# Optimization experiments

Hardware: AMD Instinct MI355X
Metric: run time of the kernel (lower is better)

Reference implementation:

```python
import jax, jax.numpy as jnp
import numpy as np

SQRT3 = float(np.sqrt(3.0))
TWO_PI = float(2.0 * np.pi)


def _safe_sqrt(x):
    return jnp.sqrt(jnp.clip(x, 1e-5))


def _matern(Q):
    # Matern 3/2 on the (already halved) quadratic form, matching torch matern()
    t = SQRT3 * _safe_sqrt(Q)
    return (1.0 + t) * jnp.exp(-t)


def _pairwise_kernel(x1, kp1, x2, kp2, scale):
    """Fused prob_product_quad + prob_product_constant + matern.

    x: [B,N,2] coords; kp: [B,N,3] = (e00, e11, e01) of SPD 2x2 E per point.
    Returns K [B,N,M].
    """
    a1, b1, c1 = kp1[..., 0], kp1[..., 1], kp1[..., 2]  # e00, e11, e01
    a2, b2, c2 = kp2[..., 0], kp2[..., 1], kp2[..., 2]
    det1 = a1 * b1 - c1 * c1  # det2x2(E1) [B,N]
    det2 = a2 * b2 - c2 * c2  # [B,M]
    s00 = a1[:, :, None] + a2[:, None, :]  # E1_00 + E2_00  [B,N,M]
    s11 = b1[:, :, None] + b2[:, None, :]
    s01 = c1[:, :, None] + c2[:, None, :]
    sdet = s00 * s11 - s01 * s01  # det(E1+E2)
    d = x1[:, :, None, :] - x2[:, None, :, :]  # [B,N,M,2]
    d0, d1 = d[..., 0], d[..., 1]
    Q = (s11 * d0 * d0 - 2.0 * s01 * d0 * d1 + s00 * d1 * d1) / sdet * 0.5
    C = 2.0 * (det1 ** 0.25)[:, :, None] * (det2 ** 0.25)[:, None, :] / _safe_sqrt(sdet)
    return _matern(Q) * C * scale


def _diag_kernel(kp, scale):
    # diagonal_prob_product: Q = 0, C = 2*sqrt(det E)/safe_sqrt(det(2E))
    a, b, c = kp[..., 0], kp[..., 1], kp[..., 2]
    det = a * b - c * c
    det2E = 4.0 * det  # det(2E) for 2x2
    C = 2.0 * jnp.sqrt(det) / _safe_sqrt(det2E)
    Q = jnp.zeros_like(C)
    return C * _matern(Q) * scale  # [B,N]


def setup_inputs() -> dict:
    key = jax.random.key(0)
    ks = jax.random.split(key, 8)
    B, N, M = 2, 1024, 16384

    def kparams(k, n):
        u = jax.random.uniform(k, (B, n, 3), dtype=jnp.float32)
        a = 0.5 + u[..., 0]
        b = 0.5 + u[..., 1]
        c = 0.2 * (u[..., 2] - 0.5)  # |c| small -> SPD
        return jnp.stack([a, b, c], axis=-1)

    coords_train = jax.random.uniform(ks[0], (B, N, 2), dtype=jnp.float32) * 512.0 / 64.0
    coords_test = jax.random.uniform(ks[1], (B, M, 2), dtype=jnp.float32) * 512.0 / 64.0
    kernel_params_train = kparams(ks[2], N)
    kernel_params_test = kparams(ks[3], M)
    y_train = jax.random.uniform(ks[4], (B, N, 1), dtype=jnp.float32) * 10.0
    var = 0.01 + 0.1 * jax.random.uniform(ks[5], (B, N), dtype=jnp.float32)
    mean = jnp.zeros((B, 1, 1), dtype=jnp.float32)
    scale_param = jnp.zeros((1,), dtype=jnp.float32)
    return {
        "coords_train": coords_train,
        "kernel_params_train": kernel_params_train,
        "coords_test": coords_test,
        "kernel_params_test": kernel_params_test,
        "y_train": y_train,
        "var": var,
        "mean": mean,
        "scale_param": scale_param,
    }


def reference(coords_train, kernel_params_train, coords_test, kernel_params_test,
              y_train, var, mean, scale_param):
    scale_prior = 1.0
    scale = scale_prior * jnp.exp(scale_param[0])  # CovarianceModule.get_scale
    B, N = coords_train.shape[0], coords_train.shape[1]

    # CovarianceModule / CrossCovarianceModule / DiagonalCovarianceModule
    K_nn = _pairwise_kernel(coords_train, kernel_params_train,
                            coords_train, kernel_params_train, scale)  # [B,N,N]
    K_nm = _pairwise_kernel(coords_train, kernel_params_train,
                            coords_test, kernel_params_test, scale)    # [B,N,M]
    K_mm_diag = _diag_kernel(kernel_params_test, scale)                 # [B,M]

    # GpSparseModule: A = K_nn + diag(var); chol; alpha = A^{-1}(y-mean); NLML
    eye = jnp.eye(N, dtype=K_nn.dtype)
    A = K_nn + var[..., None] * eye
    L = jnp.linalg.cholesky(A)
    y_centered = y_train - mean
    alpha = jax.scipy.linalg.cho_solve((L, True), y_centered)  # [B,N,1]
    data_fit = jnp.sum(y_centered * alpha, axis=1)             # [B,1]
    data_term = 0.5 * jnp.sum(data_fit, axis=1)                # [B]
    complexity_term = jnp.sum(jnp.log(jnp.diagonal(L, axis1=-2, axis2=-1)), axis=1)
    constant_term = 0.5 * N * np.log(TWO_PI)
    nlml = data_term + complexity_term + constant_term

    # GpDenseModule: predictive mean/variance at test points
    pred_mean = mean + jnp.einsum('bnm,bnk->bmk', K_nm, alpha)  # [B,M,1]
    v = jax.scipy.linalg.cho_solve((L, True), K_nm)             # [B,N,M]
    pred_var = (K_mm_diag - jnp.sum(K_nm * v, axis=1))[..., None]  # [B,M,1]
    return pred_mean, pred_var, nlml
```

## Files before the change

kernel.cpp:

```cpp
#include <hip/hip_runtime.h>
#include <math.h>

namespace {
constexpr int kB = 2;
constexpr int kN = 1024;
constexpr int kM = 16384;
constexpr float kSqrt3 = 1.7320508075688772f;

constexpr size_t A_BYTES = (size_t)kB * kN * kN * 4;
constexpr size_t DG_BYTES = (size_t)kB * 8 * 128 * 128 * 4;
constexpr size_t Z_BYTES = (size_t)kB * kN * 4;
constexpr size_t LH_BYTES = (size_t)kB * kN * kN * 2;
constexpr size_t DH_BYTES = (size_t)kB * 8 * 128 * 128 * 2;
constexpr size_t A_OFF = 0;
constexpr size_t DG_OFF = A_OFF + A_BYTES;
constexpr size_t Z_OFF = DG_OFF + DG_BYTES;
constexpr size_t LH_OFF = Z_OFF + Z_BYTES;
constexpr size_t LL_OFF = LH_OFF + LH_BYTES;
constexpr size_t DH_OFF = LL_OFF + LH_BYTES;
constexpr size_t DL_OFF = DH_OFF + DH_BYTES;
constexpr size_t WS_BYTES = DL_OFF + DH_BYTES;
}

typedef __attribute__((ext_vector_type(8))) short short8v;
typedef __attribute__((ext_vector_type(4))) float floatx4;

__device__ __forceinline__ float b16f(unsigned short h) {
  return __uint_as_float(((unsigned)h) << 16);
}
__device__ __forceinline__ unsigned short b16rn(float x) {
  unsigned u = __float_as_uint(x);
  unsigned r = u + 0x7FFFu + ((u >> 16) & 1u);
  return (unsigned short)(r >> 16);
}
__device__ __forceinline__ void split_bf16(float x, unsigned short& h, unsigned short& l) {
  unsigned u = __float_as_uint(x);
  h = (unsigned short)(u >> 16);
  float rem = x - b16f(h);
  l = (unsigned short)(__float_as_uint(rem) >> 16);
}
__device__ __forceinline__ void pack2(float v0, float v1, unsigned& hw, unsigned& lw) {
  unsigned u0 = __float_as_uint(v0), u1 = __float_as_uint(v1);
  unsigned h0 = u0 & 0xFFFF0000u;
  unsigned h1 = u1 & 0xFFFF0000u;
  hw = (h0 >> 16) | h1;
  float r0 = v0 - __uint_as_float(h0);
  float r1 = v1 - __uint_as_float(h1);
  lw = (__float_as_uint(r0) >> 16) | (__float_as_uint(r1) & 0xFFFF0000u);
}

__device__ __forceinline__ float pair_kernel(
    float x0, float x1, float a1, float b1, float c1,
    float y0, float y1, float a2, float b2, float c2, float scale) {
  float det1 = a1 * b1 - c1 * c1;
  float det2 = a2 * b2 - c2 * c2;
  float s00 = a1 + a2, s11 = b1 + b2, s01 = c1 + c2;
  float sdet = s00 * s11 - s01 * s01;
  float rsq = rsqrtf(fmaxf(sdet, 1e-5f));
  float d0 = x0 - y0, d1 = x1 - y1;
  float quad = s11 * d0 * d0 - 2.0f * s01 * d0 * d1 + s00 * d1 * d1;
  float u = 1.5f * quad * rsq * rsq;
  float t = sqrtf(fmaxf(u, 3e-5f));
  float C = 2.0f * sqrtf(sqrtf(det1)) * sqrtf(sqrtf(det2)) * rsq;
  return (1.0f + t) * __expf(-t) * C * scale;
}

__global__ __launch_bounds__(256) void build_A(
    const float* __restrict__ xt, const float* __restrict__ pt,
    const float* __restrict__ var, const float* __restrict__ sp,
    float* __restrict__ A) {
  int idx = blockIdx.x * 256 + threadIdx.x;
  int b = idx / (kN * kN);
  int r = (idx / kN) % kN;
  int c = idx % kN;
  float scale = __expf(sp[0]);
  const float* x1 = xt + ((size_t)b * kN + r) * 2;
  const float* p1 = pt + ((size_t)b * kN + r) * 3;
  const float* x2 = xt + ((size_t)b * kN + c) * 2;
  const float* p2 = pt + ((size_t)b * kN + c) * 3;
  float k = pair_kernel(x1[0], x1[1], p1[0], p1[1], p1[2],
                        x2[0], x2[1], p2[0], p2[1], p2[2], scale);
  if (r == c) k += var[b * kN + r];
  A[(size_t)idx] = k;
}

__device__ __forceinline__ void tri_decode(int idx, int& ti, int& tj) {
  float f = sqrtf(8.0f * (float)idx + 1.0f);
  int t0 = (int)((f - 1.0f) * 0.5f);
  while (t0 * (t0 + 1) / 2 > idx) --t0;
  while ((t0 + 1) * (t0 + 2) / 2 <= idx) ++t0;
  ti = t0;
  tj = idx - t0 * (t0 + 1) / 2;
}

__global__ __launch_bounds__(1024, 1) void chol_panel(float* __restrict__ A,
                                                      float* __restrict__ Dg,
                                                      unsigned short* __restrict__ Dh,
                                                      unsigned short* __restrict__ Dl, int p) {
  __shared__ float At[128 * 132];
  __shared__ float Dt[128 * 132];
  __shared__ float Tt[3 * 32 * 33];
  int b = blockIdx.x, t = threadIdx.x;
  float* Ab = A + (size_t)b * kN * kN;
  int r0 = p * 128;
#pragma unroll
  for (int q = 0; q < 4; ++q) {
    int idx = t + 1024 * q;
    int r = idx >> 5, c4 = idx & 31;
    *(float4*)&At[r * 132 + c4 * 4] = *(const float4*)&Ab[(size_t)(r0 + r) * kN + r0 + c4 * 4];
  }
  __syncthreads();
  int wave = t >> 6, lane = t & 63;
  int row0 = lane, row1 = lane + 64;
  for (int kb = 0; kb < 16; ++kb) {
    int K0 = kb * 8;
    int Kp = K0 - 8;
    if (kb > 0) {
      if (wave == 0) {
        int rr = lane >> 3, cc = lane & 7;
        float s = 0.0f;
#pragma unroll
        for (int e = 0; e < 8; ++e)
          s += At[(K0 + rr) * 132 + Kp + e] * At[(K0 + cc) * 132 + Kp + e];
        At[(K0 + rr) * 132 + K0 + cc] -= s;
      } else {
        int n = 120 - 8 * kb;
        int nt = n >> 2;
        int ntt = nt * (nt + 1) / 2;
        int base = K0 + 8;
        for (int idx = t - 64; idx < ntt; idx += 960) {
          int ti, tj;
          tri_decode(idx, ti, tj);
          int i0 = base + ti * 4, j0 = base + tj * 4;
          float Li[4][8], Lj[4][8];
#pragma unroll
          for (int r = 0; r < 4; ++r) {
            *(float4*)&Li[r][0] = *(const float4*)&At[(i0 + r) * 132 + Kp];
            *(float4*)&Li[r][4] = *(const float4*)&At[(i0 + r) * 132 + Kp + 4];
            *(float4*)&Lj[r][0] = *(const float4*)&At[(j0 + r) * 132 + Kp];
            *(float4*)&Lj[r][4] = *(const float4*)&At[(j0 + r) * 132 + Kp + 4];
          }
#pragma unroll
          for (int r = 0; r < 4; ++r) {
            float4 cv = *(const float4*)&At[(i0 + r) * 132 + j0];
            float cc4[4] = {cv.x, cv.y, cv.z, cv.w};
#pragma unroll
            for (int c = 0; c < 4; ++c) {
              float s = 0.0f;
#pragma unroll
              for (int e = 0; e < 8; ++e) s += Li[r][e] * Lj[c][e];
              cc4[c] -= s;
            }
            float4 ov = {cc4[0], cc4[1], cc4[2], cc4[3]};
            *(float4*)&At[(i0 + r) * 132 + j0] = ov;
          }
        }
      }
    }
    __syncthreads();
    if (wave == 0) {
      float rA0[8], rA1[8];
      *(float4*)&rA0[0] = *(const float4*)&At[row0 * 132 + K0];
      *(float4*)&rA0[4] = *(const float4*)&At[row0 * 132 + K0 + 4];
      *(float4*)&rA1[0] = *(const float4*)&At[row1 * 132 + K0];
      *(float4*)&rA1[4] = *(const float4*)&At[row1 * 132 + K0 + 4];
      if (kb > 0) {
        float pA0[8], pA1[8];
        *(float4*)&pA0[0] = *(const float4*)&At[row0 * 132 + Kp];
        *(float4*)&pA0[4] = *(const float4*)&At[row0 * 132 + Kp + 4];
        *(float4*)&pA1[0] = *(const float4*)&At[row1 * 132 + Kp];
        *(float4*)&pA1[4] = *(const float4*)&At[row1 * 132 + Kp + 4];
#pragma unroll
        for (int j = 0; j < 8; ++j) {
          float s0 = 0.0f, s1 = 0.0f;
#pragma unroll
          for (int e = 0; e < 8; ++e) {
            float pj = At[(K0 + j) * 132 + Kp + e];
            s0 += pA0[e] * pj;
            s1 += pA1[e] * pj;
          }
          rA0[j] -= s0;
          rA1[j] -= s1;
        }
      }
      float L11[8][8], idg[8];
#pragma unroll
      for (int r = 0; r < 8; ++r) {
        *(float4*)&L11[r][0] = *(const float4*)&At[(K0 + r) * 132 + K0];
        *(float4*)&L11[r][4] = *(const float4*)&At[(K0 + r) * 132 + K0 + 4];
      }
#pragma unroll
      for (int c = 0; c < 8; ++c) {
        float d = sqrtf(L11[c][c]);
        float iv = 1.0f / d;
        idg[c] = iv;
        L11[c][c] = d;
#pragma unroll
        for (int i = c + 1; i < 8; ++i) L11[i][c] *= iv;
#pragma unroll
        for (int j = c + 1; j < 8; ++j)
#pragma unroll
          for (int i = j; i < 8; ++i) L11[i][j] -= L11[i][c] * L11[j][c];
      }
      if (row0 >= K0 + 8) {
#pragma unroll
        for (int c = 0; c < 8; ++c) {
          float s = rA0[c];
#pragma unroll
          for (int j = 0; j < c; ++j) s -= rA0[j] * L11[c][j];
          rA0[c] = s * idg[c];
        }
      } else if (row0 >= K0) {
#pragma unroll
        for (int rr = 0; rr < 8; ++rr)
          if (row0 - K0 == rr) {
#pragma unroll
            for (int e = 0; e < 8; ++e) rA0[e] = (e <= rr) ? L11[rr][e] : 0.0f;
          }
      }
      if (row1 >= K0 + 8) {
#pragma unroll
        for (int c = 0; c < 8; ++c) {
          float s = rA1[c];
#pragma unroll
          for (int j = 0; j < c; ++j) s -= rA1[j] * L11[c][j];
          rA1[c] = s * idg[c];
        }
      } else if (row1 >= K0) {
#pragma unroll
        for (int rr = 0; rr < 8; ++rr)
          if (row1 - K0 == rr) {
#pragma unroll
            for (int e = 0; e < 8; ++e) rA1[e] = (e <= rr) ? L11[rr][e] : 0.0f;
          }
      }
      if (row0 >= K0) {
        float4 v0 = {rA0[0], rA0[1], rA0[2], rA0[3]};
        float4 v1 = {rA0[4], rA0[5], rA0[6], rA0[7]};
        *(float4*)&At[row0 * 132 + K0] = v0;
        *(float4*)&At[row0 * 132 + K0 + 4] = v1;
      }
      if (row1 >= K0) {
        float4 v0 = {rA1[0], rA1[1], rA1[2], rA1[3]};
        float4 v1 = {rA1[4], rA1[5], rA1[6], rA1[7]};
        *(float4*)&At[row1 * 132 + K0] = v0;
        *(float4*)&At[row1 * 132 + K0 + 4] = v1;
      }
    }
    __syncthreads();
  }
  if (t < 128) {
    int q = t >> 5, c = t & 31, bse = q * 32;
    float x[32];
#pragma unroll
    for (int r = 0; r < 32; ++r) {
      float s = (r == c) ? 1.0f : 0.0f;
#pragma unroll
      for (int j = 0; j < 32; ++j)
        if (j < r) s -= At[(bse + r) * 132 + bse + j] * x[j];
      x[r] = (r < c) ? 0.0f : s / At[(bse + r) * 132 + bse + r];
    }
#pragma unroll
    for (int r = 0; r < 32; ++r) Dt[(bse + r) * 132 + bse + c] = x[r];
  }
  __syncthreads();
  {
    int r = t >> 5, cl = t & 31;
    for (int s = 1; s <= 3; ++s) {
      for (int blk = 0; blk < 4 - s; ++blk) {
        int J = blk, I = J + s;
        float sum = 0.0f;
        for (int K = J; K < I; ++K)
          for (int j = 0; j < 32; ++j)
            sum += At[(I * 32 + r) * 132 + K * 32 + j] * Dt[(K * 32 + j) * 132 + J * 32 + cl];
        Tt[blk * (32 * 33) + r * 33 + cl] = sum;
      }
      __syncthreads();
      for (int blk = 0; blk < 4 - s; ++blk) {
        int J = blk, I = J + s;
        float sum = 0.0f;
        for (int j = 0; j < 32; ++j)
          sum += Dt[(I * 32 + r) * 132 + I * 32 + j] * Tt[blk * (32 * 33) + j * 33 + cl];
        Dt[(I * 32 + r) * 132 + J * 32 + cl] = -sum;
      }
      __syncthreads();
    }
  }
#pragma unroll
  for (int q = 0; q < 4; ++q) {
    int jj = t + 1024 * q;
    int r = jj >> 5, ch = jj & 31;
    int c0 = ch * 4;
    float4 v = *(const float4*)&At[r * 132 + c0];
    v.x = (c0 + 0 <= r) ? v.x : 0.0f;
    v.y = (c0 + 1 <= r) ? v.y : 0.0f;
    v.z = (c0 + 2 <= r) ? v.z : 0.0f;
    v.w = (c0 + 3 <= r) ? v.w : 0.0f;
    *(float4*)&Ab[(size_t)(r0 + r) * kN + r0 + c0] = v;
  }
  float* Db = Dg + (size_t)(b * 8 + p) * 16384;
  unsigned short* Dhb = Dh + (size_t)(b * 8 + p) * 16384;
  unsigned short* Dlb = Dl + (size_t)(b * 8 + p) * 16384;
#pragma unroll
  for (int q = 0; q < 4; ++q) {
    int jj = t + 1024 * q;
    int r = jj >> 5, ch = jj & 31;
    int c0 = ch * 4;
    float4 v = *(const float4*)&Dt[r * 132 + c0];
    v.x = (c0 + 0 <= r) ? v.x : 0.0f;
    v.y = (c0 + 1 <= r) ? v.y : 0.0f;
    v.z = (c0 + 2 <= r) ? v.z : 0.0f;
    v.w = (c0 + 3 <= r) ? v.w : 0.0f;
    *(float4*)&Db[r * 128 + c0] = v;
    float vv[4] = {v.x, v.y, v.z, v.w};
    unsigned short hs[4], ls[4];
#pragma unroll
    for (int e = 0; e < 4; ++e) split_bf16(vv[e], hs[e], ls[e]);
    *(ushort4*)&Dhb[r * 128 + c0] = make_ushort4(hs[0], hs[1], hs[2], hs[3]);
    *(ushort4*)&Dlb[r * 128 + c0] = make_ushort4(ls[0], ls[1], ls[2], ls[3]);
  }
}

__global__ __launch_bounds__(256) void chol_trsm(float* __restrict__ A,
                                                 const float* __restrict__ Dg,
                                                 unsigned short* __restrict__ Lh, int p) {
  __shared__ float At[128 * 129];
  __shared__ float Dt[128 * 129];
  int b = blockIdx.y, rb = blockIdx.x;
  int rs = (p + 1 + rb) * 128;
  float* Ab = A + (size_t)b * kN * kN;
  const float* Db = Dg + (size_t)(b * 8 + p) * 16384;
  int t = threadIdx.x;
  for (int q = 0; q < 64; ++q) {
    int li = t + 256 * q;
    int r = li >> 7, cc = li & 127;
    At[r * 129 + cc] = Ab[(size_t)(rs + r) * kN + p * 128 + cc];
    Dt[r * 129 + cc] = Db[r * 128 + cc];
  }
  __syncthreads();
  int tx = t & 15, ty = t >> 4;
  float acc[8][8] = {};
  for (int j = 0; j < 128; ++j) {
    float a[8], d[8];
#pragma unroll
    for (int q = 0; q < 8; ++q) a[q] = At[(ty * 8 + q) * 129 + j];
#pragma unroll
    for (int q = 0; q < 8; ++q) d[q] = Dt[(tx * 8 + q) * 129 + j];
#pragma unroll
    for (int qr = 0; qr < 8; ++qr)
#pragma unroll
      for (int qc = 0; qc < 8; ++qc) acc[qr][qc] = fmaf(a[qr], d[qc], acc[qr][qc]);
  }
#pragma unroll
  for (int qr = 0; qr < 8; ++qr)
#pragma unroll
    for (int qc = 0; qc < 8; ++qc) {
      float v = acc[qr][qc];
      Ab[(size_t)(rs + ty * 8 + qr) * kN + p * 128 + tx * 8 + qc] = v;
      size_t lo = ((size_t)b * kN + rs + ty * 8 + qr) * kN + p * 128 + tx * 8 + qc;
      Lh[lo] = b16rn(-v);
    }
}

__global__ __launch_bounds__(256) void chol_syrk(float* __restrict__ A, int p) {
  __shared__ float L1t[128 * 129];
  __shared__ float L2t[128 * 129];
  int b = blockIdx.y;
  int pid = blockIdx.x;
  int bi = 0;
  while ((bi + 1) * (bi + 2) / 2 <= pid) ++bi;
  int bj = pid - bi * (bi + 1) / 2;
  int rs1 = (p + 1 + bi) * 128, rs2 = (p + 1 + bj) * 128;
  float* Ab = A + (size_t)b * kN * kN;
  int t = threadIdx.x;
  for (int q = 0; q < 64; ++q) {
    int li = t + 256 * q;
    int r = li >> 7, cc = li & 127;
    L1t[r * 129 + cc] = Ab[(size_t)(rs1 + r) * kN + p * 128 + cc];
    L2t[r * 129 + cc] = Ab[(size_t)(rs2 + r) * kN + p * 128 + cc];
  }
  __syncthreads();
  int tx = t & 15, ty = t >> 4;
  float acc[8][8] = {};
  for (int j = 0; j < 128; ++j) {
    float a[8], d[8];
#pragma unroll
    for (int q = 0; q < 8; ++q) a[q] = L1t[(ty * 8 + q) * 129 + j];
#pragma unroll
    for (int q = 0; q < 8; ++q) d[q] = L2t[(tx * 8 + q) * 129 + j];
#pragma unroll
    for (int qr = 0; qr < 8; ++qr)
#pragma unroll
      for (int qc = 0; qc < 8; ++qc) acc[qr][qc] = fmaf(a[qr], d[qc], acc[qr][qc]);
  }
#pragma unroll
  for (int qr = 0; qr < 8; ++qr)
#pragma unroll
    for (int qc = 0; qc < 8; ++qc) {
      size_t o = (size_t)(rs1 + ty * 8 + qr) * kN + rs2 + tx * 8 + qc;
      Ab[o] -= acc[qr][qc];
    }
}

__global__ __launch_bounds__(1024) void solve_small(
    const float* __restrict__ A, const float* __restrict__ Dg,
    const float* __restrict__ y, const float* __restrict__ meanp,
    float* __restrict__ zbuf, float* __restrict__ out) {
  __shared__ float Ls[128 * 132];
  __shared__ __align__(16) float zs[1024];
  __shared__ float ts[128];
  __shared__ float part[128 * 9];
  __shared__ float red[1024];
  int b = blockIdx.x, t = threadIdx.x;
  int row = t & 127, g = t >> 7;
  const float* Ab = A + (size_t)b * kN * kN;
  float mv = meanp[b];
  zs[t] = y[b * kN + t] - mv;
  __syncthreads();
  for (int i = 0; i < 8; ++i) {
    float ps = 0.0f;
    for (int k = 0; k < i; ++k) {
#pragma unroll
      for (int q = 0; q < 4; ++q) {
        int li = t + 1024 * q;
        int r = li >> 5, c4 = li & 31;
        *(float4*)&Ls[r * 132 + c4 * 4] =
            *(const float4*)&Ab[(size_t)(i * 128 + r) * kN + k * 128 + c4 * 4];
      }
      __syncthreads();
      const float* Lr = &Ls[row * 132 + g * 16];
      const float* zk = &zs[k * 128 + g * 16];
#pragma unroll
      for (int c = 0; c < 16; c += 4) {
        float4 lv = *(const float4*)&Lr[c];
        float4 zv = *(const float4*)&zk[c];
        ps += lv.x * zv.x + lv.y * zv.y + lv.z * zv.z + lv.w * zv.w;
      }
      __syncthreads();
    }
    part[row * 9 + g] = ps;
    {
      const float* Db = Dg + (size_t)(b * 8 + i) * 16384;
#pragma unroll
      for (int q = 0; q < 4; ++q) {
        int li = t + 1024 * q;
        int r = li >> 5, c4 = li & 31;
        *(float4*)&Ls[r * 132 + c4 * 4] = *(const float4*)&Db[r * 128 + c4 * 4];
      }
    }
    __syncthreads();
    if (g == 0) {
      float acc = zs[i * 128 + row];
#pragma unroll
      for (int gg = 0; gg < 8; ++gg) acc -= part[row * 9 + gg];
      ts[row] = acc;
    }
    __syncthreads();
    float s = 0.0f;
    int c0 = g * 16, c1 = min(c0 + 16, row + 1);
    for (int c = c0; c < c1; ++c) s += Ls[row * 132 + c] * ts[c];
    part[row * 9 + g] = s;
    __syncthreads();
    if (g == 0) {
      float zv = 0.0f;
#pragma unroll
      for (int gg = 0; gg < 8; ++gg) zv += part[row * 9 + gg];
      zs[i * 128 + row] = zv;
    }
    __syncthreads();
  }
  red[t] = zs[t] * zs[t];
  __syncthreads();
  for (int s = 512; s > 0; s >>= 1) {
    if (t < s) red[t] += red[t + s];
    __syncthreads();
  }
  float dfs = red[0];
  __syncthreads();
  red[t] = logf(Ab[(size_t)t * kN + t]);
  __syncthreads();
  for (int s = 512; s > 0; s >>= 1) {
    if (t < s) red[t] += red[t + s];
    __syncthreads();
  }
  if (t == 0)
    out[2 * kB * kM + b] = 0.5f * dfs + red[0] + 0.5f * 1024.0f * logf(6.283185307179586f);
  zbuf[b * kN + t] = zs[t];
}

__global__ __launch_bounds__(256, 2) void fused_mfma(
    const unsigned short* __restrict__ Lh,
    const unsigned short* __restrict__ Dh, const unsigned short* __restrict__ Dl,
    const float* __restrict__ xt, const float* __restrict__ pt,
    const float* __restrict__ xs, const float* __restrict__ ps,
    const float* __restrict__ sp, const float* __restrict__ meanp,
    const float* __restrict__ zbuf, float* __restrict__ out) {
  __shared__ unsigned short Th[32 * 136];
  __shared__ unsigned short Tl[32 * 136];
  __shared__ float trp2[2][128 * 6];
  __shared__ float zs2[2][128];
  __shared__ float tp[32 * 6];
  __shared__ float red[32 * 16 * 2];
  int bid = blockIdx.x;
  int xcd = bid & 7;
  int b = xcd >> 2;
  int mt = (xcd & 3) * 128 + (bid >> 3);
  int t = threadIdx.x;
  int lane = t & 63, wave = t >> 6;
  int lrow = lane & 15, kgrp = lane >> 4;
  float scale = __expf(sp[0]);
  if (t < 32) {
    int mg = mt * 32 + t;
    float x0 = xs[((size_t)b * kM + mg) * 2 + 0];
    float x1 = xs[((size_t)b * kM + mg) * 2 + 1];
    float a = ps[((size_t)b * kM + mg) * 3 + 0];
    float bb = ps[((size_t)b * kM + mg) * 3 + 1];
    float c = ps[((size_t)b * kM + mg) * 3 + 2];
    float det2 = a * bb - c * c;
    tp[t * 6 + 0] = x0; tp[t * 6 + 1] = x1; tp[t * 6 + 2] = a;
    tp[t * 6 + 3] = bb; tp[t * 6 + 4] = c; tp[t * 6 + 5] = sqrtf(sqrtf(det2));
  }
  if (t < 128) {
    size_t n = (size_t)b * kN + t;
    float x0 = xt[n * 2 + 0];
    float x1 = xt[n * 2 + 1];
    float a = pt[n * 3 + 0];
    float bb = pt[n * 3 + 1];
    float c = pt[n * 3 + 2];
    float det1 = a * bb - c * c;
    trp2[0][t * 6 + 0] = x0; trp2[0][t * 6 + 1] = x1; trp2[0][t * 6 + 2] = a;
    trp2[0][t * 6 + 3] = bb; trp2[0][t * 6 + 4] = c;
    trp2[0][t * 6 + 5] = 2.0f * scale * sqrtf(sqrtf(det1));
    zs2[0][t] = zbuf[n];
  }
  floatx4 W[8][2][2];
#pragma unroll
  for (int i = 0; i < 8; ++i)
#pragma unroll
    for (int rf = 0; rf < 2; ++rf)
#pragma unroll
      for (int cf = 0; cf < 2; ++cf) W[i][rf][cf] = (floatx4){0.f, 0.f, 0.f, 0.f};
  float pma[2] = {0.f, 0.f}, s2a[2] = {0.f, 0.f};
  __syncthreads();

#define FUSED_K_STEP(KC)                                                                   \
  {                                                                                        \
    constexpr int k = (KC);                                                                \
    const float* trp = trp2[k & 1];                                                        \
                                                           \
    _Pragma("unroll")                                                                      \
    for (int rf = 0; rf < 2; ++rf) {                                                       \
      int n0 = wave * 32 + rf * 16 + kgrp * 4;                                             \
      float nx0[4], nx1[4], na[4], nb[4], nc[4], nc1[4];                                   \
      _Pragma("unroll")                                                                    \
      for (int r = 0; r < 4; ++r) {                                                        \
        int n = n0 + r;                                                                    \
        nx0[r] = trp[n * 6 + 0]; nx1[r] = trp[n * 6 + 1]; na[r] = trp[n * 6 + 2];          \
        nb[r] = trp[n * 6 + 3]; nc[r] = trp[n * 6 + 4]; nc1[r] = trp[n * 6 + 5];           \
      }                                                                                    \
      _Pragma("unroll")                                                                    \
      for (int cf = 0; cf < 2; ++cf) {                                                     \
        int m = cf * 16 + lrow;                                                            \
        float mx0 = tp[m * 6 + 0], mx1 = tp[m * 6 + 1], ma = tp[m * 6 + 2];                \
        float mb = tp[m * 6 + 3], mc = tp[m * 6 + 4], mq = tp[m * 6 + 5];                  \
        float Tv[4];                                                                       \
        _Pragma("unroll")                                                                  \
        for (int r = 0; r < 4; ++r) {                                                      \
          float s00 = na[r] + ma, s11 = nb[r] + mb, s01 = nc[r] + mc;                      \
          float sdet = s00 * s11 - s01 * s01;                                              \
          float rsq = rsqrtf(fmaxf(sdet, 1e-5f));                                          \
          float d0 = nx0[r] - mx0, d1 = nx1[r] - mx1;                                      \
          float quad = s11 * d0 * d0 - 2.0f * s01 * d0 * d1 + s00 * d1 * d1;               \
          float u = 1.5f * quad * rsq * rsq;                                               \
          float tt = sqrtf(fmaxf(u, 3e-5f));                                               \
          float Kv = (1.0f + tt) * __expf(-tt) * nc1[r] * (mq * rsq);                      \
          Tv[r] = Kv + W[k][rf][cf][r];                                                    \
        }                                                                                  \
        unsigned hw[2], lw[2];                                                             \
        pack2(Tv[0], Tv[1], hw[0], lw[0]);                                                 \
        pack2(Tv[2], Tv[3], hw[1], lw[1]);                                                 \
        int off = m * 136 + n0;                                                            \
        *(uint2*)&Th[off] = make_uint2(hw[0], hw[1]);                                      \
        *(uint2*)&Tl[off] = make_uint2(lw[0], lw[1]);                                      \
      }                                                                                    \
    }                                                                                      \
    __syncthreads();                                                                \
                                 \
    if (k < 7 && t < 128) {                                                                \
      size_t n = (size_t)b * kN + (k + 1) * 128 + t;                                       \
      float x0 = xt[n * 2 + 0];                                                            \
      float x1 = xt[n * 2 + 1];                                                            \
      float a = pt[n * 3 + 0];                                                             \
      float bb = pt[n * 3 + 1];                                                            \
      float c = pt[n * 3 + 2];                                                             \
      float det1 = a * bb - c * c;                                                         \
      trp2[(k + 1) & 1][t * 6 + 0] = x0; trp2[(k + 1) & 1][t * 6 + 1] = x1;                \
      trp2[(k + 1) & 1][t * 6 + 2] = a;  trp2[(k + 1) & 1][t * 6 + 3] = bb;                \
      trp2[(k + 1) & 1][t * 6 + 4] = c;                                                    \
      trp2[(k + 1) & 1][t * 6 + 5] = 2.0f * scale * sqrtf(sqrtf(det1));                    \
      zs2[(k + 1) & 1][t] = zbuf[n];                                                       \
    }                                                                                      \
    floatx4 wk[2][2];                                                                      \
    _Pragma("unroll")                                                                      \
    for (int rf = 0; rf < 2; ++rf)                                                         \
      _Pragma("unroll")                                                                    \
      for (int cf = 0; cf < 2; ++cf) wk[rf][cf] = (floatx4){0.f, 0.f, 0.f, 0.f};           \
    {                                                                                      \
      const unsigned short* Dhb = Dh + (size_t)(b * 8 + k) * 16384;                        \
      const unsigned short* Dlb = Dl + (size_t)(b * 8 + k) * 16384;                        \
      _Pragma("unroll")                                                                    \
      for (int ks = 0; ks < 4; ++ks) {                                                     \
        short8v bh[2], bl[2];                                                              \
        _Pragma("unroll")                                                                  \
        for (int cf = 0; cf < 2; ++cf) {                                                   \
          int boff = (cf * 16 + lrow) * 136 + ks * 32 + kgrp * 8;                          \
          bh[cf] = *(const short8v*)&Th[boff];                                             \
          bl[cf] = *(const short8v*)&Tl[boff];                                             \
        }                                                                                  \
        short8v ah[2], al[2];                                                              \
        _Pragma("unroll")                                                                  \
        for (int rf = 0; rf < 2; ++rf) {                                                   \
          size_t aoff = (size_t)(wave * 32 + rf * 16 + lrow) * 128 + ks * 32 + kgrp * 8;   \
          ah[rf] = *(const short8v*)&Dhb[aoff];                                            \
          al[rf] = *(const short8v*)&Dlb[aoff];                                            \
        }                                                                                  \
        _Pragma("unroll")                                                                  \
        for (int rf = 0; rf < 2; ++rf)                                                     \
          _Pragma("unroll")                                                                \
          for (int cf = 0; cf < 2; ++cf) {                                                 \
            wk[rf][cf] = __builtin_amdgcn_mfma_f32_16x16x32_bf16(ah[rf], bh[cf], wk[rf][cf], 0, 0, 0); \
            wk[rf][cf] = __builtin_amdgcn_mfma_f32_16x16x32_bf16(ah[rf], bl[cf], wk[rf][cf], 0, 0, 0); \
            wk[rf][cf] = __builtin_amdgcn_mfma_f32_16x16x32_bf16(al[rf], bh[cf], wk[rf][cf], 0, 0, 0); \
          }                                                                                \
      }                                                                                    \
    }                                                                                      \
    __syncthreads();                                                                \
                                               \
    _Pragma("unroll")                                                                      \
    for (int rf = 0; rf < 2; ++rf) {                                                       \
      int n0 = wave * 32 + rf * 16 + kgrp * 4;                                             \
      _Pragma("unroll")                                                                    \
      for (int cf = 0; cf < 2; ++cf) {                                                     \
        int m = cf * 16 + lrow;                                                            \
        float wv[4];                                                                       \
        _Pragma("unroll")                                                                  \
        for (int r = 0; r < 4; ++r) {                                                      \
          wv[r] = wk[rf][cf][r];                                                           \
          pma[cf] = fmaf(wv[r], zs2[k & 1][n0 + r], pma[cf]);                              \
          s2a[cf] = fmaf(wv[r], wv[r], s2a[cf]);                                           \
        }                                                                                  \
        unsigned hw[2], lw[2];                                                             \
        pack2(wv[0], wv[1], hw[0], lw[0]);                                                 \
        pack2(wv[2], wv[3], hw[1], lw[1]);                                                 \
        int off = m * 136 + n0;                                                            \
        *(uint2*)&Th[off] = make_uint2(hw[0], hw[1]);                                      \
        *(uint2*)&Tl[off] = make_uint2(lw[0], lw[1]);                                      \
      }                                                                                    \
    }                                                                                      \
    __syncthreads();                                                                \
                                                            \
    __builtin_amdgcn_s_setprio(1);                                                         \
    _Pragma("unroll")                                                                      \
    for (int ks = 0; ks < 4; ++ks) {                                                       \
      short8v bh[2], bl[2];                                                                \
      _Pragma("unroll")                                                                    \
      for (int cf = 0; cf < 2; ++cf) {                                                     \
        int boff = (cf * 16 + lrow) * 136 + ks * 32 + kgrp * 8;                            \
        bh[cf] = *(const short8v*)&Th[boff];                                               \
        bl[cf] = *(const short8v*)&Tl[boff];                                               \
      }                                                                                    \
      _Pragma("unroll")                                                                    \
      for (int i = k + 1; i < 8; ++i) {                                                    \
        short8v ah[2];                                                                     \
        _Pragma("unroll")                                                                  \
        for (int rf = 0; rf < 2; ++rf) {                                                   \
          size_t ro = (size_t)b * kN + i * 128 + wave * 32 + rf * 16 + lrow;               \
          size_t aoff = ro * kN + k * 128 + ks * 32 + kgrp * 8;                            \
          ah[rf] = *(const short8v*)&Lh[aoff];                                             \
        }                                                                                  \
        _Pragma("unroll")                                                                  \
        for (int rf = 0; rf < 2; ++rf)                                                     \
          _Pragma("unroll")                                                                \
          for (int cf = 0; cf < 2; ++cf) {                                                 \
            W[i][rf][cf] = __builtin_amdgcn_mfma_f32_16x16x32_bf16(ah[rf], bh[cf], W[i][rf][cf], 0, 0, 0); \
            W[i][rf][cf] = __builtin_amdgcn_mfma_f32_16x16x32_bf16(ah[rf], bl[cf], W[i][rf][cf], 0, 0, 0); \
          }                                                                                \
      }                                                                                    \
    }                                                                                      \
    __builtin_amdgcn_s_setprio(0);                                                         \
    __syncthreads();             \
  }

  FUSED_K_STEP(0)
  FUSED_K_STEP(1)
  FUSED_K_STEP(2)
  FUSED_K_STEP(3)
  FUSED_K_STEP(4)
  FUSED_K_STEP(5)
  FUSED_K_STEP(6)
  FUSED_K_STEP(7)
#undef FUSED_K_STEP

#pragma unroll
  for (int cf = 0; cf < 2; ++cf) {
    int m = cf * 16 + lrow;
    red[m * 16 + wave * 4 + kgrp] = pma[cf];
    red[512 + m * 16 + wave * 4 + kgrp] = s2a[cf];
  }
  __syncthreads();
  if (t < 32) {
    float pm = 0.f, s2 = 0.f;
#pragma unroll
    for (int j = 0; j < 16; ++j) {
      pm += red[t * 16 + j];
      s2 += red[512 + t * 16 + j];
    }
    int mg = mt * 32 + t;
    float a = tp[t * 6 + 2], bb = tp[t * 6 + 3], c = tp[t * 6 + 4];
    float det = a * bb - c * c;
    float C = 2.0f * sqrtf(det) * rsqrtf(fmaxf(4.0f * det, 1e-5f));
    float t0 = kSqrt3 * sqrtf(1e-5f);
    float mat = (1.0f + t0) * __expf(-t0);
    float kd = C * mat * scale;
    out[b * kM + mg] = meanp[b] + pm;
    out[kB * kM + b * kM + mg] = kd - s2;
  }
}

extern "C" void kernel_launch(void* const* d_in, const int* in_sizes, int n_in,
                              void* d_out, int out_size, void* d_ws, size_t ws_size,
                              hipStream_t stream) {
  const float* xt = (const float*)d_in[0];
  const float* pt = (const float*)d_in[1];
  const float* xs = (const float*)d_in[2];
  const float* ps = (const float*)d_in[3];
  const float* y = (const float*)d_in[4];
  const float* var = (const float*)d_in[5];
  const float* meanp = (const float*)d_in[6];
  const float* sp = (const float*)d_in[7];
  float* out = (float*)d_out;
  char* ws = (char*)d_ws;
  if (ws_size < WS_BYTES) return;

  float* A = (float*)(ws + A_OFF);
  float* Dg = (float*)(ws + DG_OFF);
  float* zbuf = (float*)(ws + Z_OFF);
  unsigned short* Lh = (unsigned short*)(ws + LH_OFF);
  unsigned short* Dh = (unsigned short*)(ws + DH_OFF);
  unsigned short* Dl = (unsigned short*)(ws + DL_OFF);

  build_A<<<(kB * kN * kN) / 256, 256, 0, stream>>>(xt, pt, var, sp, A);
  for (int p = 0; p < 8; ++p) {
    chol_panel<<<kB, 1024, 0, stream>>>(A, Dg, Dh, Dl, p);
    if (p < 7) {
      int nt = 7 - p;
      chol_trsm<<<dim3(nt, kB), 256, 0, stream>>>(A, Dg, Lh, p);
      chol_syrk<<<dim3(nt * (nt + 1) / 2, kB), 256, 0, stream>>>(A, p);
    }
  }
  solve_small<<<kB, 1024, 0, stream>>>(A, Dg, y, meanp, zbuf, out);
  fused_mfma<<<kB * 512, 256, 0, stream>>>(Lh, Dh, Dl, xt, pt, xs, ps,
                                           sp, meanp, zbuf, out);
}
```

Baseline: 1.135 ms.

## Fuse blocked Cholesky panel/trsm/syrk launches into one cooperative kernel

Replaces the 22 separate panel, trsm and syrk kernel launches with a single cooperative kernel of 56 blocks that uses grid-wide syncs between stages. Each block takes a batch and a role: panel factor, a trsm row block, or a syrk tile pair. The goal is to remove per-launch overhead and tail gaps in the serial Cholesky chain. In exchange, trsm and syrk now run as 1024-thread blocks with 4x4 register tiles instead of 256 threads with 8x8, and grid.sync carries its own barrier cost.

Measured after the change: 1.338 ms. 17.9% more time.

```diff
diff --git a/kernel.cpp b/kernel.cpp
--- a/kernel.cpp
+++ b/kernel.cpp
@@ -1,5 +1,8 @@
 #include <hip/hip_runtime.h>
+#include <hip/hip_cooperative_groups.h>
 #include <math.h>
+
+namespace cg = cooperative_groups;
 
 namespace {
 constexpr int kB = 2;
@@ -20,6 +23,12 @@
 constexpr size_t DH_OFF = LL_OFF + LH_BYTES;
 constexpr size_t DL_OFF = DH_OFF + DH_BYTES;
 constexpr size_t WS_BYTES = DL_OFF + DH_BYTES;
+
+constexpr int PAN_AT = 0;
+constexpr int PAN_DT = 16896;
+constexpr int PAN_TT = 33792;
+constexpr int PAN_FLOATS = 36960;
+constexpr int GEMM_B = 16512;
 }
 
 typedef __attribute__((ext_vector_type(8))) short short8v;
@@ -93,16 +102,12 @@
   tj = idx - t0 * (t0 + 1) / 2;
 }
 
-__global__ __launch_bounds__(1024, 1) void chol_panel(float* __restrict__ A,
-                                                      float* __restrict__ Dg,
-                                                      unsigned short* __restrict__ Dh,
-                                                      unsigned short* __restrict__ Dl, int p) {
-  __shared__ float At[128 * 132];
-  __shared__ float Dt[128 * 132];
-  __shared__ float Tt[3 * 32 * 33];
-  int b = blockIdx.x, t = threadIdx.x;
-  float* Ab = A + (size_t)b * kN * kN;
-  int r0 = p * 128;
+__device__ void panel_factor_1024(float* __restrict__ sh, float* __restrict__ Ab,
+                                  float* __restrict__ Db, unsigned short* __restrict__ Dhb,
+                                  unsigned short* __restrict__ Dlb, int r0, int t) {
+  float* At = sh + PAN_AT;
+  float* Dt = sh + PAN_DT;
+  float* Tt = sh + PAN_TT;
 #pragma unroll
   for (int q = 0; q < 4; ++q) {
     int idx = t + 1024 * q;
@@ -298,9 +303,6 @@
     v.w = (c0 + 3 <= r) ? v.w : 0.0f;
     *(float4*)&Ab[(size_t)(r0 + r) * kN + r0 + c0] = v;
   }
-  float* Db = Dg + (size_t)(b * 8 + p) * 16384;
-  unsigned short* Dhb = Dh + (size_t)(b * 8 + p) * 16384;
-  unsigned short* Dlb = Dl + (size_t)(b * 8 + p) * 16384;
 #pragma unroll
   for (int q = 0; q < 4; ++q) {
     int jj = t + 1024 * q;
@@ -321,85 +323,104 @@
   }
 }
 
-__global__ __launch_bounds__(256) void chol_trsm(float* __restrict__ A,
-                                                 const float* __restrict__ Dg,
-                                                 unsigned short* __restrict__ Lh, int p) {
-  __shared__ float At[128 * 129];
-  __shared__ float Dt[128 * 129];
-  int b = blockIdx.y, rb = blockIdx.x;
-  int rs = (p + 1 + rb) * 128;
+__global__ __launch_bounds__(1024, 1) void chol_coop(
+    float* __restrict__ A, float* __restrict__ Dg,
+    unsigned short* __restrict__ Dh, unsigned short* __restrict__ Dl,
+    unsigned short* __restrict__ Lh) {
+  cg::grid_group grid = cg::this_grid();
+  __shared__ float sh[PAN_FLOATS];
+  int wid = blockIdx.x;
+  int t = threadIdx.x;
+  int b = wid & 1;
+  int role = wid >> 1;
   float* Ab = A + (size_t)b * kN * kN;
-  const float* Db = Dg + (size_t)(b * 8 + p) * 16384;
-  int t = threadIdx.x;
-  for (int q = 0; q < 64; ++q) {
-    int li = t + 256 * q;
-    int r = li >> 7, cc = li & 127;
-    At[r * 129 + cc] = Ab[(size_t)(rs + r) * kN + p * 128 + cc];
-    Dt[r * 129 + cc] = Db[r * 128 + cc];
-  }
-  __syncthreads();
-  int tx = t & 15, ty = t >> 4;
-  float acc[8][8] = {};
-  for (int j = 0; j < 128; ++j) {
-    float a[8], d[8];
-#pragma unroll
-    for (int q = 0; q < 8; ++q) a[q] = At[(ty * 8 + q) * 129 + j];
-#pragma unroll
-    for (int q = 0; q < 8; ++q) d[q] = Dt[(tx * 8 + q) * 129 + j];
-#pragma unroll
-    for (int qr = 0; qr < 8; ++qr)
-#pragma unroll
-      for (int qc = 0; qc < 8; ++qc) acc[qr][qc] = fmaf(a[qr], d[qc], acc[qr][qc]);
-  }
-#pragma unroll
-  for (int qr = 0; qr < 8; ++qr)
-#pragma unroll
-    for (int qc = 0; qc < 8; ++qc) {
-      float v = acc[qr][qc];
-      Ab[(size_t)(rs + ty * 8 + qr) * kN + p * 128 + tx * 8 + qc] = v;
-      size_t lo = ((size_t)b * kN + rs + ty * 8 + qr) * kN + p * 128 + tx * 8 + qc;
-      Lh[lo] = b16rn(-v);
-    }
-}
-
-__global__ __launch_bounds__(256) void chol_syrk(float* __restrict__ A, int p) {
-  __shared__ float L1t[128 * 129];
-  __shared__ float L2t[128 * 129];
-  int b = blockIdx.y;
-  int pid = blockIdx.x;
-  int bi = 0;
-  while ((bi + 1) * (bi + 2) / 2 <= pid) ++bi;
-  int bj = pid - bi * (bi + 1) / 2;
-  int rs1 = (p + 1 + bi) * 128, rs2 = (p + 1 + bj) * 128;
-  float* Ab = A + (size_t)b * kN * kN;
-  int t = threadIdx.x;
-  for (int q = 0; q < 64; ++q) {
-    int li = t + 256 * q;
-    int r = li >> 7, cc = li & 127;
-    L1t[r * 129 + cc] = Ab[(size_t)(rs1 + r) * kN + p * 128 + cc];
-    L2t[r * 129 + cc] = Ab[(size_t)(rs2 + r) * kN + p * 128 + cc];
-  }
-  __syncthreads();
-  int tx = t & 15, ty = t >> 4;
-  float acc[8][8] = {};
-  for (int j = 0; j < 128; ++j) {
-    float a[8], d[8];
-#pragma unroll
-    for (int q = 0; q < 8; ++q) a[q] = L1t[(ty * 8 + q) * 129 + j];
-#pragma unroll
-    for (int q = 0; q < 8; ++q) d[q] = L2t[(tx * 8 + q) * 129 + j];
-#pragma unroll
-    for (int qr = 0; qr < 8; ++qr)
-#pragma unroll
-      for (int qc = 0; qc < 8; ++qc) acc[qr][qc] = fmaf(a[qr], d[qc], acc[qr][qc]);
-  }
-#pragma unroll
-  for (int qr = 0; qr < 8; ++qr)
-#pragma unroll
-    for (int qc = 0; qc < 8; ++qc) {
-      size_t o = (size_t)(rs1 + ty * 8 + qr) * kN + rs2 + tx * 8 + qc;
-      Ab[o] -= acc[qr][qc];
-    }
+  if (role == 0)
+    panel_factor_1024(sh, Ab, Dg + (size_t)(b * 8) * 16384,
+                      Dh + (size_t)(b * 8) * 16384, Dl + (size_t)(b * 8) * 16384, 0, t);
+  grid.sync();
+  for (int p = 0; p < 7; ++p) {
+    int nt = 7 - p;
+    if (role < nt) {
+      float* At = sh;
+      float* Dt = sh + GEMM_B;
+      const float* Db = Dg + (size_t)(b * 8 + p) * 16384;
+      int rs = (p + 1 + role) * 128;
+#pragma unroll
+      for (int q = 0; q < 16; ++q) {
+        int li = t + 1024 * q;
+        int r = li >> 7, cc = li & 127;
+        At[r * 129 + cc] = Ab[(size_t)(rs + r) * kN + p * 128 + cc];
+        Dt[r * 129 + cc] = Db[r * 128 + cc];
+      }
+      __syncthreads();
+      int tx = t & 31, ty = t >> 5;
+      float acc[4][4] = {};
+      for (int j = 0; j < 128; ++j) {
+        float a[4], d[4];
+#pragma unroll
+        for (int q = 0; q < 4; ++q) a[q] = At[(ty * 4 + q) * 129 + j];
+#pragma unroll
+        for (int q = 0; q < 4; ++q) d[q] = Dt[(tx * 4 + q) * 129 + j];
+#pragma unroll
+        for (int qr = 0; qr < 4; ++qr)
+#pragma unroll
+          for (int qc = 0; qc < 4; ++qc) acc[qr][qc] = fmaf(a[qr], d[qc], acc[qr][qc]);
+      }
+#pragma unroll
+      for (int qr = 0; qr < 4; ++qr)
+#pragma unroll
+        for (int qc = 0; qc < 4; ++qc) {
+          float v = acc[qr][qc];
+          Ab[(size_t)(rs + ty * 4 + qr) * kN + p * 128 + tx * 4 + qc] = v;
+          size_t lo = ((size_t)b * kN + rs + ty * 4 + qr) * kN + p * 128 + tx * 4 + qc;
+          Lh[lo] = b16rn(-v);
+        }
+    }
+    grid.sync();
+    int npairs = nt * (nt + 1) / 2;
+    if (role < npairs) {
+      float* L1t = sh;
+      float* L2t = sh + GEMM_B;
+      int bi = 0;
+      while ((bi + 1) * (bi + 2) / 2 <= role) ++bi;
+      int bj = role - bi * (bi + 1) / 2;
+      int rs1 = (p + 1 + bi) * 128, rs2 = (p + 1 + bj) * 128;
+#pragma unroll
+      for (int q = 0; q < 16; ++q) {
+        int li = t + 1024 * q;
+        int r = li >> 7, cc = li & 127;
+        L1t[r * 129 + cc] = Ab[(size_t)(rs1 + r) * kN + p * 128 + cc];
+        L2t[r * 129 + cc] = Ab[(size_t)(rs2 + r) * kN + p * 128 + cc];
+      }
+      __syncthreads();
+      int tx = t & 31, ty = t >> 5;
+      float acc[4][4] = {};
+      for (int j = 0; j < 128; ++j) {
+        float a[4], d[4];
+#pragma unroll
+        for (int q = 0; q < 4; ++q) a[q] = L1t[(ty * 4 + q) * 129 + j];
+#pragma unroll
+        for (int q = 0; q < 4; ++q) d[q] = L2t[(tx * 4 + q) * 129 + j];
+#pragma unroll
+        for (int qr = 0; qr < 4; ++qr)
+#pragma unroll
+          for (int qc = 0; qc < 4; ++qc) acc[qr][qc] = fmaf(a[qr], d[qc], acc[qr][qc]);
+      }
+#pragma unroll
+      for (int qr = 0; qr < 4; ++qr)
+#pragma unroll
+        for (int qc = 0; qc < 4; ++qc) {
+          size_t o = (size_t)(rs1 + ty * 4 + qr) * kN + rs2 + tx * 4 + qc;
+          Ab[o] -= acc[qr][qc];
+        }
+    }
+    grid.sync();
+    if (role == 0)
+      panel_factor_1024(sh, Ab, Dg + (size_t)(b * 8 + p + 1) * 16384,
+                        Dh + (size_t)(b * 8 + p + 1) * 16384,
+                        Dl + (size_t)(b * 8 + p + 1) * 16384, (p + 1) * 128, t);
+    grid.sync();
+  }
 }
 
 __global__ __launch_bounds__(1024) void solve_small(
@@ -750,13 +771,9 @@
   unsigned short* Dl = (unsigned short*)(ws + DL_OFF);
 
   build_A<<<(kB * kN * kN) / 256, 256, 0, stream>>>(xt, pt, var, sp, A);
-  for (int p = 0; p < 8; ++p) {
-    chol_panel<<<kB, 1024, 0, stream>>>(A, Dg, Dh, Dl, p);
-    if (p < 7) {
-      int nt = 7 - p;
-      chol_trsm<<<dim3(nt, kB), 256, 0, stream>>>(A, Dg, Lh, p);
-      chol_syrk<<<dim3(nt * (nt + 1) / 2, kB), 256, 0, stream>>>(A, p);
-    }
+  {
+    void* kargs[] = {(void*)&A, (void*)&Dg, (void*)&Dh, (void*)&Dl, (void*)&Lh};
+    hipLaunchCooperativeKernel((void*)chol_coop, dim3(56), dim3(1024), kargs, 0, stream);
   }
   solve_small<<<kB, 1024, 0, stream>>>(A, Dg, y, meanp, zbuf, out);
   fused_mfma<<<kB * 512, 256, 0, stream>>>(Lh, Dh, Dl, xt, pt, xs, ps,
```
